# Kernel optimization log

Hardware: AMD Instinct MI355X
Metric: run time of the kernel (lower is better)

The kernel has to match this reference:

```python
import jax, jax.numpy as jnp
import numpy as np

LAYERS, HIDDEN, FFN, HEADS = 4, 128, 256, 4
HEAD_D = HIDDEN // HEADS          # 32
V_HEAD = 2 * HEAD_D               # 64 (double_v_dim)
V_DIM = 2 * HIDDEN                # 256
SCALE_BASE = 512
EPS = 1e-5
GAMMAS = (1.0 - np.exp(np.linspace(np.log(1.0 / 32), np.log(1.0 / 512), HEADS))).astype(np.float32)


def _xpos(x, downscale):
    # x: (..., L, d) -- xpos rotary embedding with per-position decay scale
    L, d = x.shape[-2], x.shape[-1]
    half = d // 2
    base_scale = (jnp.arange(half, dtype=jnp.float32) + 0.4 * d) / (1.4 * d)   # (half,)
    power = jnp.arange(L, dtype=jnp.float32)[:, None] / SCALE_BASE
    sc = base_scale[None, :] ** power                                          # (L, half)
    inv_freq = 1.0 / (10000.0 ** (jnp.arange(half, dtype=jnp.float32) / half))
    ang = jnp.arange(L, dtype=jnp.float32)[:, None] * inv_freq[None, :]        # (L, half)
    sin, cos = jnp.sin(ang), jnp.cos(ang)
    if downscale:
        sc = 1.0 / sc
    sin_d = jnp.repeat(sin * sc, 2, axis=-1)   # duplicate_interleave -> (L, d)
    cos_d = jnp.repeat(cos * sc, 2, axis=-1)
    x1, x2 = x[..., ::2], x[..., 1::2]
    rot = jnp.stack((-x2, x1), axis=-1).reshape(x.shape)  # rotate_every_two
    return x * cos_d + rot * sin_d


def _layer_norm(x, w, b):
    mu = x.mean(-1, keepdims=True)
    var = x.var(-1, keepdims=True)
    return (x - mu) / jnp.sqrt(var + EPS) * w + b


def _msr(X, wq, wk, wv, wg, wo, gn_w, gn_b):
    # MultiScaleRetention, parallel form. X: (B, L, HIDDEN)
    B, L, _ = X.shape
    Q = _xpos(jnp.einsum('blh,nhd->bnld', X, wq), False)   # (B, heads, L, 32)
    K = _xpos(jnp.einsum('blh,nhd->bnld', X, wk), True)
    V = jnp.einsum('blh,nhv->bnlv', X, wv)                 # (B, heads, L, 64)
    n = jnp.arange(L)
    diff = n[:, None] - n[None, :]
    gam = jnp.asarray(GAMMAS)[:, None, None]
    D = jnp.where(diff >= 0, gam ** jnp.maximum(diff, 0).astype(jnp.float32), 0.0)  # (heads, L, L)
    scores = jnp.einsum('bnld,bnmd->bnlm', Q, K) * D[None]
    Y = jnp.einsum('bnlm,bnmv->bnlv', scores, V)
    Y = Y.transpose(0, 2, 1, 3).reshape(B, L, V_DIM)       # concat heads on feature dim
    # GroupNorm(heads, V_DIM) over the channel axis
    Yg = Y.reshape(B, L, HEADS, V_HEAD)
    mu = Yg.mean(-1, keepdims=True)
    var = Yg.var(-1, keepdims=True)
    Yn = ((Yg - mu) / jnp.sqrt(var + EPS)).reshape(B, L, V_DIM) * gn_w + gn_b
    G = X @ wg
    return (G * jax.nn.sigmoid(G) * Yn) @ wo               # swish gate, output proj


def _forward(x, rem_w1, rem_b1, rem_w2, rem_b2, rem_w3, rem_b3,
             wq, wk, wv, wg, wo, gn_w, gn_b,
             ln1_w, ln1_b, ln2_w, ln2_b,
             ffn_w1, ffn_b1, ffn_w2, ffn_b2,
             dec_w1, dec_b1, dec_w2, dec_b2):
    gelu = lambda t: jax.nn.gelu(t, approximate=False)
    # REM: 5 -> 32 -> 64 -> 128, GELU after each linear
    X = gelu(gelu(gelu(x @ rem_w1 + rem_b1) @ rem_w2 + rem_b2) @ rem_w3 + rem_b3)
    # RetNet: pre-LN retention + pre-LN FFN blocks with residuals
    for i in range(LAYERS):
        Y = _msr(_layer_norm(X, ln1_w[i], ln1_b[i]), wq[i], wk[i], wv[i],
                 wg[i], wo[i], gn_w[i], gn_b[i]) + X
        Z = _layer_norm(Y, ln2_w[i], ln2_b[i])
        X = gelu(Z @ ffn_w1[i] + ffn_b1[i]) @ ffn_w2[i] + ffn_b2[i] + Y
    # Decoder: 128 -> 64 -> 20, softmax over classes
    logits = gelu(X @ dec_w1 + dec_b1) @ dec_w2 + dec_b2
    return jax.nn.softmax(logits, axis=-1)


def setup_inputs() -> dict:
    key = jax.random.key(0)
    ks = jax.random.split(key, 16)
    rn = lambda k, shape, s=0.02: jax.random.normal(k, shape, dtype=jnp.float32) * s
    B, L = 64, 512
    return {
        'x': jax.random.normal(ks[0], (B, L, 5), dtype=jnp.float32),
        'rem_w1': rn(ks[1], (5, 32)), 'rem_b1': jnp.zeros((32,), jnp.float32),
        'rem_w2': rn(ks[2], (32, 64)), 'rem_b2': jnp.zeros((64,), jnp.float32),
        'rem_w3': rn(ks[3], (64, HIDDEN)), 'rem_b3': jnp.zeros((HIDDEN,), jnp.float32),
        'wq': rn(ks[4], (LAYERS, HEADS, HIDDEN, HEAD_D), 1.0 / HIDDEN),
        'wk': rn(ks[5], (LAYERS, HEADS, HIDDEN, HEAD_D), 1.0 / HIDDEN),
        'wv': rn(ks[6], (LAYERS, HEADS, HIDDEN, V_HEAD), 1.0 / HIDDEN),
        'wg': rn(ks[7], (LAYERS, HIDDEN, V_DIM), 1.0 / HIDDEN),
        'wo': rn(ks[8], (LAYERS, V_DIM, HIDDEN), 1.0 / HIDDEN),
        'gn_w': jnp.ones((LAYERS, V_DIM), jnp.float32),
        'gn_b': jnp.zeros((LAYERS, V_DIM), jnp.float32),
        'ln1_w': jnp.ones((LAYERS, HIDDEN), jnp.float32),
        'ln1_b': jnp.zeros((LAYERS, HIDDEN), jnp.float32),
        'ln2_w': jnp.ones((LAYERS, HIDDEN), jnp.float32),
        'ln2_b': jnp.zeros((LAYERS, HIDDEN), jnp.float32),
        'ffn_w1': rn(ks[9], (LAYERS, HIDDEN, FFN)),
        'ffn_b1': jnp.zeros((LAYERS, FFN), jnp.float32),
        'ffn_w2': rn(ks[10], (LAYERS, FFN, HIDDEN)),
        'ffn_b2': jnp.zeros((LAYERS, HIDDEN), jnp.float32),
        'dec_w1': rn(ks[11], (HIDDEN, 64)), 'dec_b1': jnp.zeros((64,), jnp.float32),
        'dec_w2': rn(ks[12], (64, 20)), 'dec_b2': jnp.zeros((20,), jnp.float32),
    }


def reference(x, rem_w1, rem_b1, rem_w2, rem_b2, rem_w3, rem_b3,
              wq, wk, wv, wg, wo, gn_w, gn_b,
              ln1_w, ln1_b, ln2_w, ln2_b,
              ffn_w1, ffn_b1, ffn_w2, ffn_b2,
              dec_w1, dec_b1, dec_w2, dec_b2):
    return _forward(x, rem_w1, rem_b1, rem_w2, rem_b2, rem_w3, rem_b3,
                    wq, wk, wv, wg, wo, gn_w, gn_b,
                    ln1_w, ln1_b, ln2_w, ln2_b,
                    ffn_w1, ffn_b1, ffn_w2, ffn_b2,
                    dec_w1, dec_b1, dec_w2, dec_b2)
```

## Files before the change

kernel.cpp:

```cpp
#include <hip/hip_runtime.h>
#include <math.h>
#include <cmath>

#define SEQ   512
#define NBATCH 64
#define BT    32768
#define HID   128
#define NHEAD 4
#define HD    32
#define VHD   64
#define VDIM  256
#define FFND  256

typedef __attribute__((ext_vector_type(8))) short bf16x8;
typedef __attribute__((ext_vector_type(4))) float f32x4;
typedef unsigned short u16;

__device__ __forceinline__ float gelu_f(float x){ return 0.5f*x*(1.f+erff(x*0.70710678118f)); }

__device__ __forceinline__ u16 f2bf(float f){
  __bf16 h = (__bf16)f;
  union{__bf16 h; u16 u;} v; v.h = h; return v.u;
}
__device__ __forceinline__ float bf2f(u16 u){
  union{unsigned u; float f;} v; v.u = ((unsigned)u)<<16; return v.f;
}

__device__ __forceinline__ void gload16(const void* g, void* l){
  __builtin_amdgcn_global_load_lds(
      (const __attribute__((address_space(1))) unsigned*)g,
      (__attribute__((address_space(3))) unsigned*)l, 16, 0, 0);
}

#define STAGE_TILE_N(dst, base, strideU16, colOffU16, wid_, srow_, phys16l_, NIT) \
  do{                                                                           \
    _Pragma("unroll")                                                           \
    for(int it_=0; it_<NIT; it_++){                                             \
      int blk_ = (wid_)*NIT + it_;                                              \
      int row_ = blk_*4 + (srow_);                                              \
      int log16_ = (phys16l_) ^ (row_&15);                                      \
      gload16((base) + (size_t)row_*(strideU16) + (colOffU16) + log16_*8,       \
              &(dst)[blk_*512]);                                                \
    }                                                                           \
  }while(0)

#define STAGE_TILE(dst, base, strideU16, colOffU16, wid_, srow_, phys16l_) \
  STAGE_TILE_N(dst, base, strideU16, colOffU16, wid_, srow_, phys16l_, 8)

__global__ __launch_bounds__(256) void wconv_kernel(
    const float* __restrict__ wq, const float* __restrict__ wk,
    const float* __restrict__ wv, const float* __restrict__ wg,
    const float* __restrict__ wo, const float* __restrict__ f1,
    const float* __restrict__ f2, const float* __restrict__ dw1,
    const float* __restrict__ w2e, const float* __restrict__ w3e,
    u16* __restrict__ Wt)
{
  int idx = blockIdx.x*256 + threadIdx.x;
  if(idx >= 786432){
    int q = idx - 786432;
    if(q < 8192){ int col=q>>7, h=q&127; Wt[idx]=f2bf(dw1[h*64+col]); }
    else if(q < 10240){ int p=q-8192; int row=p>>5, col=p&31; Wt[idx]=f2bf(w2e[col*64+row]); }
    else { int p=q-10240; int row=p>>6, col=p&63; Wt[idx]=f2bf(w3e[col*128+row]); }
    return;
  }
  int layer = idx / 196608;
  int r = idx - layer*196608;
  u16* W = Wt + (size_t)layer*196608;
  const float* wq_l = wq + (size_t)layer*16384;
  const float* wk_l = wk + (size_t)layer*16384;
  const float* wv_l = wv + (size_t)layer*32768;
  const float* wg_l = wg + (size_t)layer*32768;
  const float* wo_l = wo + (size_t)layer*32768;
  const float* f1_l = f1 + (size_t)layer*32768;
  const float* f2_l = f2 + (size_t)layer*32768;
  float v;
  if(r < 98304){
    int col = r>>7, h = r&127;
    if(col<128){ int n=col>>5, d=col&31; v = wq_l[(n*128+h)*32+d]; }
    else if(col<256){ int c=col-128, n=c>>5, d=c&31; v = wk_l[(n*128+h)*32+d]; }
    else if(col<512){ int c=col-256, n=c>>6, j=c&63; v = wv_l[(n*128+h)*64+j]; }
    else { int p=col-512; v = wg_l[h*256+p]; }
    W[r] = f2bf(v);
  } else if(r < 131072){
    int q = r-98304; int col=q>>8, k=q&255;
    W[r] = f2bf(wo_l[k*128+col]);
  } else if(r < 163840){
    int q = r-131072; int col=q>>7, h=q&127;
    W[r] = f2bf(f1_l[h*256+col]);
  } else {
    int q = r-163840; int col=q>>8, k=q&255;
    W[r] = f2bf(f2_l[k*128+col]);
  }
}

__global__ __launch_bounds__(256) void embed_kernel(
    const float* __restrict__ x,
    const float* __restrict__ w1, const float* __restrict__ b1,
    const float* __restrict__ b2, const float* __restrict__ b3,
    const u16* __restrict__ W23t,
    const float* __restrict__ lnw, const float* __restrict__ lnb,
    float* __restrict__ X, u16* __restrict__ xn)
{
  __shared__ float sx[64][6];
  __shared__ float sw1[160], sb1[32], sb2[64], sb3[128];
  __shared__ u16 big[18944];
  int t=threadIdx.x, lane=t&63, wid=t>>6, mrow=lane&15, quad=lane>>4, r0=wid*16;
  int tok0=blockIdx.x*64;

  for(int i=t;i<320;i+=256) sx[i/5][i%5]=x[(size_t)tok0*5+i];
  for(int i=t;i<160;i+=256) sw1[i]=w1[i];
  if(t<32) sb1[t]=b1[t];
  if(t<64) sb2[t]=b2[t];
  if(t<128) sb3[t]=b3[t];
  for(int c=t;c<256;c+=256){ int row=c>>2, c8=(c&3)*8;
    *(uint4*)&big[2560+row*40+c8]=*(const uint4*)&W23t[row*32+c8]; }
  for(int c=t;c<1024;c+=256){ int row=c>>3, c8=(c&7)*8;
    *(uint4*)&big[9728+row*72+c8]=*(const uint4*)&W23t[2048+row*64+c8]; }
  __syncthreads();

  for(int task=t; task<2048; task+=256){
    int tok=task>>5, j=task&31;
    float a=sb1[j];
    #pragma unroll
    for(int i=0;i<5;i++) a+=sx[tok][i]*sw1[i*32+j];
    big[tok*40+j]=f2bf(gelu_f(a));
  }
  __syncthreads();

  f32x4 h2[4];
  #pragma unroll
  for(int cc=0;cc<4;cc++) h2[cc]=(f32x4){0.f,0.f,0.f,0.f};
  {
    bf16x8 a=*(const bf16x8*)&big[(r0+mrow)*40+quad*8];
    #pragma unroll
    for(int cc=0;cc<4;cc++){
      bf16x8 b=*(const bf16x8*)&big[2560+(cc*16+mrow)*40+quad*8];
      h2[cc]=__builtin_amdgcn_mfma_f32_16x16x32_bf16(a,b,h2[cc],0,0,0);
    }
  }
  #pragma unroll
  for(int cc=0;cc<4;cc++){
    float bs=sb2[cc*16+mrow];
    #pragma unroll
    for(int reg=0;reg<4;reg++)
      big[5120+(r0+quad*4+reg)*72+cc*16+mrow]=f2bf(gelu_f(h2[cc][reg]+bs));
  }
  __syncthreads();

  f32x4 xac[8];
  #pragma unroll
  for(int cc=0;cc<8;cc++) xac[cc]=(f32x4){0.f,0.f,0.f,0.f};
  #pragma unroll
  for(int ks=0;ks<2;ks++){
    bf16x8 a=*(const bf16x8*)&big[5120+(r0+mrow)*72+ks*32+quad*8];
    #pragma unroll
    for(int cc=0;cc<8;cc++){
      bf16x8 b=*(const bf16x8*)&big[9728+(cc*16+mrow)*72+ks*32+quad*8];
      xac[cc]=__builtin_amdgcn_mfma_f32_16x16x32_bf16(a,b,xac[cc],0,0,0);
    }
  }
  __syncthreads();

  #pragma unroll
  for(int reg=0;reg<4;reg++){
    int rowl=r0+quad*4+reg, rowg=tok0+rowl;
    float xv[8], s=0.f, sq=0.f;
    #pragma unroll
    for(int cc=0;cc<8;cc++){
      float v=gelu_f(xac[cc][reg]+sb3[cc*16+mrow]);
      xv[cc]=v; s+=v; sq+=v*v;
    }
    #pragma unroll
    for(int m=1;m<16;m<<=1){ s+=__shfl_xor(s,m); sq+=__shfl_xor(sq,m); }
    float mu=s*(1.f/128.f);
    float var=sq*(1.f/128.f)-mu*mu;
    float rstd=rsqrtf(var+1e-5f);
    #pragma unroll
    for(int cc=0;cc<8;cc++){
      int col=cc*16+mrow;
      X[(size_t)rowg*128+col]=xv[cc];
      big[rowl*136+col]=f2bf((xv[cc]-mu)*rstd*lnw[col]+lnb[col]);
    }
  }
  __syncthreads();
  for(int th=t; th<1024; th+=256){
    int row=th>>4, seg=th&15;
    *(uint4*)&xn[(size_t)(tok0+row)*128+seg*8]=*(const uint4*)&big[row*136+seg*8];
  }
}

__device__ __forceinline__ void qkvg_epilogue(
    int nc, f32x4 acc[2][4], u16* stg,
    int t, int mrow, int quad, int r0q, int c0q, int b, int l0, int tok0,
    u16* __restrict__ Q, u16* __restrict__ K,
    u16* __restrict__ Vt, u16* __restrict__ G)
{
  if(nc < 2){
    bool isK = (nc==1);
    float sgn = isK ? -1.f : 1.f;
    #pragma unroll
    for(int cc=0;cc<4;cc++){
      int colc = c0q + cc*16 + mrow;
      int i = (colc&31)>>1;
      float log2bs = log2f(((float)i + 12.8f)*(1.f/44.8f));
      float invf   = exp2f(-(float)i * (13.28771238f/16.f));
      float rstep  = exp2f(sgn*log2bs*(1.f/512.f));
      float c1 = cosf(invf), s1 = sinf(invf);
      #pragma unroll
      for(int rr=0;rr<2;rr++){
        int rowl0 = r0q + rr*16 + quad*4;
        float lb = (float)(l0 + rowl0);
        float sc = exp2f(sgn*log2bs*lb*(1.f/512.f));
        float ang = lb*invf;
        float u = cosf(ang)*sc, v = sinf(ang)*sc;
        #pragma unroll
        for(int reg=0;reg<4;reg++){
          int rowl = rowl0 + reg;
          float val = acc[rr][cc][reg];
          float partner = __shfl_xor(val, 1);
          float o = (colc&1) ? (val*u + partner*v) : (val*u - partner*v);
          stg[rowl*136 + colc] = f2bf(o);
          float un = (u*c1 - v*s1)*rstep;
          float vn = (u*s1 + v*c1)*rstep;
          u = un; v = vn;
        }
      }
    }
    __syncthreads();
    u16* O = isK ? K : Q;
    for(int th=t; th<1024; th+=256){
      int row=th>>4, n=(th>>2)&3, seg=th&3;
      *(uint4*)&O[(((size_t)(b*4+n)*512) + (l0+row))*32 + seg*8]
        = *(const uint4*)&stg[row*136 + n*32 + seg*8];
    }
  } else if(nc < 4){
    #pragma unroll
    for(int cc=0;cc<4;cc++){
      int colc = c0q + cc*16 + mrow;
      #pragma unroll
      for(int rr=0;rr<2;rr++){
        #pragma unroll
        for(int reg=0;reg<4;reg++){
          int rowl = r0q + rr*16 + quad*4 + reg;
          stg[colc*72 + rowl] = f2bf(acc[rr][cc][reg]);
        }
      }
    }
    __syncthreads();
    int jbase = (nc-2)*128;
    for(int th=t; th<1024; th+=256){
      int row=th>>3, seg=th&7;
      int jg = jbase + row; int n = jg>>6, j = jg&63;
      *(uint4*)&Vt[(((size_t)(b*4+n)*64) + j)*512 + l0 + seg*8]
        = *(const uint4*)&stg[row*72 + seg*8];
    }
  } else {
    #pragma unroll
    for(int cc=0;cc<4;cc++){
      int colc = c0q + cc*16 + mrow;
      #pragma unroll
      for(int rr=0;rr<2;rr++){
        #pragma unroll
        for(int reg=0;reg<4;reg++){
          int rowl = r0q + rr*16 + quad*4 + reg;
          stg[rowl*136 + colc] = f2bf(acc[rr][cc][reg]);
        }
      }
    }
    __syncthreads();
    int gc0 = (nc-4)*128;
    for(int th=t; th<1024; th+=256){
      int row=th>>4, seg=th&15;
      *(uint4*)&G[((size_t)(tok0+row))*256 + gc0 + seg*8]
        = *(const uint4*)&stg[row*136 + seg*8];
    }
  }
}

__device__ __forceinline__ void qkvg_epi8(
    int nc, f32x4 acc[4], u16* stg,
    int t, int mrow, int quad, int r0, int c0, int b, int l0, int tok0,
    u16* __restrict__ Q, u16* __restrict__ K,
    u16* __restrict__ Vt, u16* __restrict__ G)
{
  if(nc < 2){
    bool isK = (nc==1);
    float sgn = isK ? -1.f : 1.f;
    #pragma unroll
    for(int cc=0;cc<4;cc++){
      int colc = c0 + cc*16 + mrow;
      int i = (colc&31)>>1;
      float log2bs = log2f(((float)i + 12.8f)*(1.f/44.8f));
      float invf   = exp2f(-(float)i * (13.28771238f/16.f));
      float rstep  = exp2f(sgn*log2bs*(1.f/512.f));
      float c1 = cosf(invf), s1 = sinf(invf);
      int rowl0 = r0 + quad*4;
      float lb = (float)(l0 + rowl0);
      float sc = exp2f(sgn*log2bs*lb*(1.f/512.f));
      float ang = lb*invf;
      float u = cosf(ang)*sc, v = sinf(ang)*sc;
      #pragma unroll
      for(int reg=0;reg<4;reg++){
        int rowl = rowl0 + reg;
        float val = acc[cc][reg];
        float partner = __shfl_xor(val, 1);
        float o = (colc&1) ? (val*u + partner*v) : (val*u - partner*v);
        stg[rowl*136 + colc] = f2bf(o);
        float un = (u*c1 - v*s1)*rstep;
        float vn = (u*s1 + v*c1)*rstep;
        u = un; v = vn;
      }
    }
    __syncthreads();
    u16* O = isK ? K : Q;
    for(int th=t; th<1024; th+=512){
      int row=th>>4, n=(th>>2)&3, seg=th&3;
      *(uint4*)&O[(((size_t)(b*4+n)*512) + (l0+row))*32 + seg*8]
        = *(const uint4*)&stg[row*136 + n*32 + seg*8];
    }
  } else if(nc < 4){
    #pragma unroll
    for(int cc=0;cc<4;cc++){
      int colc = c0 + cc*16 + mrow;
      #pragma unroll
      for(int reg=0;reg<4;reg++){
        int rowl = r0 + quad*4 + reg;
        stg[colc*72 + rowl] = f2bf(acc[cc][reg]);
      }
    }
    __syncthreads();
    int jbase = (nc-2)*128;
    for(int th=t; th<1024; th+=512){
      int row=th>>3, seg=th&7;
      int jg = jbase + row; int n = jg>>6, j = jg&63;
      *(uint4*)&Vt[(((size_t)(b*4+n)*64) + j)*512 + l0 + seg*8]
        = *(const uint4*)&stg[row*72 + seg*8];
    }
  } else {
    #pragma unroll
    for(int cc=0;cc<4;cc++){
      int colc = c0 + cc*16 + mrow;
      #pragma unroll
      for(int reg=0;reg<4;reg++){
        int rowl = r0 + quad*4 + reg;
        stg[rowl*136 + colc] = f2bf(acc[cc][reg]);
      }
    }
    __syncthreads();
    int gc0 = (nc-4)*128;
    for(int th=t; th<1024; th+=512){
      int row=th>>4, seg=th&15;
      *(uint4*)&G[((size_t)(tok0+row))*256 + gc0 + seg*8]
        = *(const uint4*)&stg[row*136 + seg*8];
    }
  }
}

__global__ __launch_bounds__(256) void qkvg_kernel(
    const u16* __restrict__ A, const u16* __restrict__ Wt,
    u16* __restrict__ Q, u16* __restrict__ K,
    u16* __restrict__ Vt, u16* __restrict__ G)
{
  __shared__ u16 sW[128*128];
  u16* stg = sW;
  int t = threadIdx.x, lane = t&63, wid = t>>6;
  int mrow = lane&15, quad = lane>>4;
  int srow = lane>>4, phys16l = lane&15;
  int r0q = (wid>>1)*32, c0q = (wid&1)*64;
  int tok0 = blockIdx.x*64;
  int b = tok0>>9, l0 = tok0&511;

  bf16x8 a0f[4], a1f[4];
  #pragma unroll
  for(int ks=0; ks<4; ks++){
    a0f[ks] = *(const bf16x8*)&A[(size_t)(tok0+r0q+mrow)*128 + ks*32+quad*8];
    a1f[ks] = *(const bf16x8*)&A[(size_t)(tok0+r0q+16+mrow)*128 + ks*32+quad*8];
  }

  for(int ch=0; ch<3; ch++){
    int nc = blockIdx.y*3 + ch;
    if(ch) __syncthreads();
    STAGE_TILE(sW, Wt + (size_t)nc*16384, 128, 0, wid, srow, phys16l);
    __syncthreads();

    f32x4 acc[2][4];
    #pragma unroll
    for(int rr=0;rr<2;rr++)
      #pragma unroll
      for(int cc=0;cc<4;cc++) acc[rr][cc] = (f32x4){0.f,0.f,0.f,0.f};
    #pragma unroll
    for(int ks=0; ks<4; ks++){
      #pragma unroll
      for(int cc=0; cc<4; cc++){
        bf16x8 bb = *(const bf16x8*)&sW[(c0q+cc*16+mrow)*128 + (((ks*4+quad)^mrow)<<3)];
        acc[0][cc] = __builtin_amdgcn_mfma_f32_16x16x32_bf16(a0f[ks],bb,acc[0][cc],0,0,0);
        acc[1][cc] = __builtin_amdgcn_mfma_f32_16x16x32_bf16(a1f[ks],bb,acc[1][cc],0,0,0);
      }
    }
    __syncthreads();
    qkvg_epilogue(nc, acc, stg, t, mrow, quad, r0q, c0q, b, l0, tok0, Q, K, Vt, G);
  }
}

__global__ __launch_bounds__(512, 4) void mlpq_kernel(
    const u16* __restrict__ Gated, const u16* __restrict__ Wo,
    const u16* __restrict__ W1t, const float* __restrict__ b1,
    const u16* __restrict__ W2t, const float* __restrict__ b2,
    const float* __restrict__ Xin,
    const float* __restrict__ ln2w, const float* __restrict__ ln2b,
    const float* __restrict__ ln1w, const float* __restrict__ ln1b,
    float* __restrict__ Xout,
    const u16* __restrict__ Wq,
    u16* __restrict__ Q, u16* __restrict__ K,
    u16* __restrict__ Vt, u16* __restrict__ G)
{
  __shared__ u16 sW[32768];
  __shared__ float sRed[64][2][2];
  u16* bufA = sW;
  u16* bufB = sW + 16384;
  int t=threadIdx.x, lane=t&63, wid=t>>6, mrow=lane&15, quad=lane>>4;
  int rg=wid>>1, half=wid&1;
  int r0=rg*16, c0=half*64;
  int tok0=blockIdx.x*64;
  int srow = lane>>4, phys16l = lane&15;

  STAGE_TILE_N(bufA, Wo, 256, 0, wid, srow, phys16l, 4);
  bf16x8 gfrag[8];
  #pragma unroll
  for(int ks=0;ks<8;ks++)
    gfrag[ks]=*(const bf16x8*)&Gated[(size_t)(tok0+r0+mrow)*256 + ks*32+quad*8];
  __syncthreads();

  STAGE_TILE_N(bufB, Wo, 256, 128, wid, srow, phys16l, 4);
  f32x4 yac[4];
  #pragma unroll
  for(int cc=0;cc<4;cc++) yac[cc]=(f32x4){0.f,0.f,0.f,0.f};
  #pragma unroll
  for(int cc=0;cc<4;cc++){
    #pragma unroll
    for(int ks=0;ks<4;ks++){
      bf16x8 b=*(const bf16x8*)&bufA[(c0+cc*16+mrow)*128 + (((ks*4+quad)^mrow)<<3)];
      yac[cc]=__builtin_amdgcn_mfma_f32_16x16x32_bf16(gfrag[ks],b,yac[cc],0,0,0);
    }
  }
  __syncthreads();

  STAGE_TILE_N(bufA, W1t, 128, 0, wid, srow, phys16l, 4);
  #pragma unroll
  for(int cc=0;cc<4;cc++){
    #pragma unroll
    for(int ks=0;ks<4;ks++){
      bf16x8 b=*(const bf16x8*)&bufB[(c0+cc*16+mrow)*128 + (((ks*4+quad)^mrow)<<3)];
      yac[cc]=__builtin_amdgcn_mfma_f32_16x16x32_bf16(gfrag[4+ks],b,yac[cc],0,0,0);
    }
  }
  float yv[4][4];
  #pragma unroll
  for(int reg=0;reg<4;reg++){
    int rowl=r0+quad*4+reg, rowg=tok0+rowl;
    float s=0.f, sq=0.f;
    #pragma unroll
    for(int cc=0;cc<4;cc++){
      float v=yac[cc][reg]+Xin[(size_t)rowg*128+c0+cc*16+mrow];
      yv[cc][reg]=v; s+=v; sq+=v*v;
    }
    #pragma unroll
    for(int m=1;m<16;m<<=1){ s+=__shfl_xor(s,m); sq+=__shfl_xor(sq,m); }
    if(mrow==0){ sRed[rowl][half][0]=s; sRed[rowl][half][1]=sq; }
  }
  __syncthreads();

  #pragma unroll
  for(int reg=0;reg<4;reg++){
    int rowl=r0+quad*4+reg;
    float s =sRed[rowl][0][0]+sRed[rowl][1][0];
    float sq=sRed[rowl][0][1]+sRed[rowl][1][1];
    float mu=s*(1.f/128.f);
    float var=sq*(1.f/128.f)-mu*mu;
    float rstd=rsqrtf(var+1e-5f);
    #pragma unroll
    for(int cc=0;cc<4;cc++){
      int col=c0+cc*16+mrow;
      bufB[rowl*136+col]=f2bf((yv[cc][reg]-mu)*rstd*ln2w[col]+ln2b[col]);
    }
  }
  __syncthreads();
  bf16x8 az[4];
  #pragma unroll
  for(int ks=0;ks<4;ks++) az[ks]=*(const bf16x8*)&bufB[(r0+mrow)*136+ks*32+quad*8];
  __syncthreads();

  bf16x8 hfrag[8];
  STAGE_TILE_N(bufB, W1t + (size_t)16384, 128, 0, wid, srow, phys16l, 4);
  {
    f32x4 hac[4];
    #pragma unroll
    for(int cc=0;cc<4;cc++) hac[cc]=(f32x4){0.f,0.f,0.f,0.f};
    #pragma unroll
    for(int cc=0;cc<4;cc++){
      #pragma unroll
      for(int ks=0;ks<4;ks++){
        bf16x8 b=*(const bf16x8*)&bufA[(c0+cc*16+mrow)*128 + (((ks*4+quad)^mrow)<<3)];
        hac[cc]=__builtin_amdgcn_mfma_f32_16x16x32_bf16(az[ks],b,hac[cc],0,0,0);
      }
    }
    __syncthreads();
    #pragma unroll
    for(int cc=0;cc<4;cc++){
      float bs=b1[c0+cc*16+mrow];
      #pragma unroll
      for(int reg=0;reg<4;reg++)
        bufA[(r0+quad*4+reg)*136 + c0+cc*16+mrow]=f2bf(gelu_f(hac[cc][reg]+bs));
    }
    __syncthreads();
    #pragma unroll
    for(int ks=0;ks<4;ks++) hfrag[ks]=*(const bf16x8*)&bufA[(r0+mrow)*136+ks*32+quad*8];
    __syncthreads();
  }

  STAGE_TILE_N(bufA, W2t, 256, 0, wid, srow, phys16l, 4);
  {
    f32x4 hac[4];
    #pragma unroll
    for(int cc=0;cc<4;cc++) hac[cc]=(f32x4){0.f,0.f,0.f,0.f};
    #pragma unroll
    for(int cc=0;cc<4;cc++){
      #pragma unroll
      for(int ks=0;ks<4;ks++){
        bf16x8 b=*(const bf16x8*)&bufB[(c0+cc*16+mrow)*128 + (((ks*4+quad)^mrow)<<3)];
        hac[cc]=__builtin_amdgcn_mfma_f32_16x16x32_bf16(az[ks],b,hac[cc],0,0,0);
      }
    }
    __syncthreads();
    #pragma unroll
    for(int cc=0;cc<4;cc++){
      float bs=b1[128+c0+cc*16+mrow];
      #pragma unroll
      for(int reg=0;reg<4;reg++)
        bufB[(r0+quad*4+reg)*136 + c0+cc*16+mrow]=f2bf(gelu_f(hac[cc][reg]+bs));
    }
    __syncthreads();
    #pragma unroll
    for(int ks=0;ks<4;ks++) hfrag[4+ks]=*(const bf16x8*)&bufB[(r0+mrow)*136+ks*32+quad*8];
    __syncthreads();
  }

  STAGE_TILE_N(bufB, W2t, 256, 128, wid, srow, phys16l, 4);
  f32x4 xac[4];
  #pragma unroll
  for(int cc=0;cc<4;cc++) xac[cc]=(f32x4){0.f,0.f,0.f,0.f};
  #pragma unroll
  for(int cc=0;cc<4;cc++){
    #pragma unroll
    for(int ks=0;ks<4;ks++){
      bf16x8 b=*(const bf16x8*)&bufA[(c0+cc*16+mrow)*128 + (((ks*4+quad)^mrow)<<3)];
      xac[cc]=__builtin_amdgcn_mfma_f32_16x16x32_bf16(hfrag[ks],b,xac[cc],0,0,0);
    }
  }
  __syncthreads();

  if(Wq) STAGE_TILE_N(bufA, Wq, 128, 0, wid, srow, phys16l, 4);
  #pragma unroll
  for(int cc=0;cc<4;cc++){
    #pragma unroll
    for(int ks=0;ks<4;ks++){
      bf16x8 b=*(const bf16x8*)&bufB[(c0+cc*16+mrow)*128 + (((ks*4+quad)^mrow)<<3)];
      xac[cc]=__builtin_amdgcn_mfma_f32_16x16x32_bf16(hfrag[4+ks],b,xac[cc],0,0,0);
    }
  }
  float xv[4][4];
  #pragma unroll
  for(int reg=0;reg<4;reg++){
    int rowl=r0+quad*4+reg;
    float s=0.f, sq=0.f;
    #pragma unroll
    for(int cc=0;cc<4;cc++){
      float v=xac[cc][reg]+b2[c0+cc*16+mrow]+yv[cc][reg];
      xv[cc][reg]=v; s+=v; sq+=v*v;
    }
    #pragma unroll
    for(int m=1;m<16;m<<=1){ s+=__shfl_xor(s,m); sq+=__shfl_xor(sq,m); }
    if(mrow==0){ sRed[rowl][half][0]=s; sRed[rowl][half][1]=sq; }
  }
  __syncthreads();

  #pragma unroll
  for(int reg=0;reg<4;reg++){
    int rowl=r0+quad*4+reg, rowg=tok0+rowl;
    float s =sRed[rowl][0][0]+sRed[rowl][1][0];
    float sq=sRed[rowl][0][1]+sRed[rowl][1][1];
    float mu=s*(1.f/128.f);
    float var=sq*(1.f/128.f)-mu*mu;
    float rstd=rsqrtf(var+1e-5f);
    #pragma unroll
    for(int cc=0;cc<4;cc++){
      int col=c0+cc*16+mrow;
      Xout[(size_t)rowg*128+col]=xv[cc][reg];
      if(Wq) bufB[rowl*136+col]=f2bf((xv[cc][reg]-mu)*rstd*ln1w[col]+ln1b[col]);
    }
  }
  if(!Wq) return;
  __syncthreads();
  bf16x8 aq[4];
  #pragma unroll
  for(int ks=0; ks<4; ks++)
    aq[ks] = *(const bf16x8*)&bufB[(r0+mrow)*136 + ks*32+quad*8];
  __syncthreads();

  int b = tok0>>9, l0 = tok0&511;
  for(int nc=0; nc<6; nc++){
    u16* cur = (nc&1) ? bufB : bufA;
    u16* nxt = (nc&1) ? bufA : bufB;
    if(nc<5) STAGE_TILE_N(nxt, Wq + (size_t)(nc+1)*16384, 128, 0, wid, srow, phys16l, 4);

    f32x4 acc[4];
    #pragma unroll
    for(int cc=0;cc<4;cc++) acc[cc] = (f32x4){0.f,0.f,0.f,0.f};
    #pragma unroll
    for(int ks=0; ks<4; ks++){
      #pragma unroll
      for(int cc=0; cc<4; cc++){
        bf16x8 bb = *(const bf16x8*)&cur[(c0+cc*16+mrow)*128 + (((ks*4+quad)^mrow)<<3)];
        acc[cc] = __builtin_amdgcn_mfma_f32_16x16x32_bf16(aq[ks],bb,acc[cc],0,0,0);
      }
    }
    __syncthreads();
    qkvg_epi8(nc, acc, cur, t, mrow, quad, r0, c0, b, l0, tok0, Q, K, Vt, G);
    __syncthreads();
  }
}

__global__ __launch_bounds__(256) void retmfma_kernel(
    const u16* __restrict__ Q, const u16* __restrict__ K,
    const u16* __restrict__ Vt, const u16* __restrict__ G,
    const float* __restrict__ gnw, const float* __restrict__ gnb,
    u16* __restrict__ Gated, float4 log2g)
{
  int idx = blockIdx.x;
  int bn = ((idx>>6)<<3) | (idx&7);
  int lt = (idx>>3)&7;
  int n = bn & 3, b = bn >> 2;
  float lg2g = (n==0)?log2g.x:(n==1)?log2g.y:(n==2)?log2g.z:log2g.w;
  __shared__ u16 sK[64][40];
  __shared__ u16 sVt[64][72];
  __shared__ u16 sS[64][72];
  int t = threadIdx.x, lane = t&63, wid = t>>6;
  int mrow = lane&15, quad = lane>>4;
  int r0 = wid*16;

  bf16x8 qa = *(const bf16x8*)&Q[((size_t)bn*512 + lt*64 + r0+mrow)*32 + quad*8];

  f32x4 oacc[4];
  #pragma unroll
  for(int cc=0;cc<4;cc++) oacc[cc] = (f32x4){0.f,0.f,0.f,0.f};
  float gp1 = exp2f(lg2g), gp2 = gp1*gp1, gp3 = gp2*gp1;
  float gpow[4] = {1.f, gp1, gp2, gp3};
  float gw[4], gb[4];
  #pragma unroll
  for(int cc=0;cc<4;cc++){ gw[cc]=gnw[n*64+cc*16+mrow]; gb[cc]=gnb[n*64+cc*16+mrow]; }
  int rowl0 = lt*64 + r0 + quad*4;

  int krow = t>>2, kc8 = (t&3)*8;
  int vrow = t>>3, vc8 = (t&7)*8;
  const u16* Kb = K  + ((size_t)bn*512 + krow)*32 + kc8;
  const u16* V0 = Vt + ((size_t)bn*64 + vrow)*512 + vc8;
  const u16* V1 = Vt + ((size_t)bn*64 + vrow+32)*512 + vc8;
  uint4 ldk  = *(const uint4*)(Kb);
  uint4 ldv0 = *(const uint4*)(V0);
  uint4 ldv1 = *(const uint4*)(V1);

  for(int mt=0; mt<=lt; mt++){
    if(mt) __syncthreads();
    *(uint4*)&sK[krow][kc8]     = ldk;
    *(uint4*)&sVt[vrow][vc8]    = ldv0;
    *(uint4*)&sVt[vrow+32][vc8] = ldv1;
    if(mt < lt){
      ldk  = *(const uint4*)(Kb + (size_t)(mt+1)*2048);
      ldv0 = *(const uint4*)(V0 + (mt+1)*64);
      ldv1 = *(const uint4*)(V1 + (mt+1)*64);
    }
    __syncthreads();
    f32x4 sacc[4];
    #pragma unroll
    for(int cc=0;cc<4;cc++){
      bf16x8 bb = *(const bf16x8*)&sK[cc*16+mrow][quad*8];
      sacc[cc] = __builtin_amdgcn_mfma_f32_16x16x32_bf16(qa,bb,(f32x4){0.f,0.f,0.f,0.f},0,0,0);
    }
    #pragma unroll
    for(int cc=0;cc<4;cc++){
      int colm = mt*64 + cc*16 + mrow;
      int d0 = rowl0 - colm;
      float w0 = exp2f(lg2g*(float)d0);
      #pragma unroll
      for(int reg=0;reg<4;reg++){
        float w = (d0+reg>=0) ? w0*gpow[reg] : 0.f;
        sS[r0+quad*4+reg][cc*16+mrow] = f2bf(sacc[cc][reg]*w);
      }
    }
    __syncthreads();
    #pragma unroll
    for(int ks=0;ks<2;ks++){
      bf16x8 a = *(const bf16x8*)&sS[r0+mrow][ks*32+quad*8];
      #pragma unroll
      for(int cc=0;cc<4;cc++){
        bf16x8 bb = *(const bf16x8*)&sVt[cc*16+mrow][ks*32+quad*8];
        oacc[cc] = __builtin_amdgcn_mfma_f32_16x16x32_bf16(a,bb,oacc[cc],0,0,0);
      }
    }
  }

  __syncthreads();
  #pragma unroll
  for(int reg=0;reg<4;reg++){
    float s=0.f, sq=0.f;
    #pragma unroll
    for(int cc=0;cc<4;cc++){ float v=oacc[cc][reg]; s+=v; sq+=v*v; }
    #pragma unroll
    for(int m=1;m<16;m<<=1){ s+=__shfl_xor(s,m); sq+=__shfl_xor(sq,m); }
    float mu = s*(1.f/64.f);
    float var = sq*(1.f/64.f) - mu*mu;
    float rn = rsqrtf(var + 1e-5f);
    int rowl = r0 + quad*4 + reg;
    int l = lt*64 + rowl;
    size_t gbase = ((size_t)(b*512 + l))*256 + n*64;
    #pragma unroll
    for(int cc=0;cc<4;cc++){
      float gg = bf2f(G[gbase + cc*16+mrow]);
      float gate = gg/(1.f+expf(-gg));
      sS[rowl][cc*16+mrow] = f2bf(gate*((oacc[cc][reg]-mu)*rn*gw[cc] + gb[cc]));
    }
  }
  __syncthreads();
  for(int th=t; th<512; th+=256){
    int row=th>>3, seg=th&7;
    *(uint4*)&Gated[((size_t)(b*512 + lt*64 + row))*256 + n*64 + seg*8]
      = *(const uint4*)&sS[row][seg*8];
  }
}

__global__ __launch_bounds__(256) void dec_kernel(
    const float* __restrict__ X, const u16* __restrict__ W1t,
    const float* __restrict__ b1, const float* __restrict__ w2,
    const float* __restrict__ b2, float* __restrict__ out)
{
  __shared__ u16 sA[64][136];
  __shared__ u16 sW[64][136];
  __shared__ float sH[64][68];
  __shared__ float sL[64*20];
  __shared__ float sw2[64*20];
  __shared__ float sb2[20];
  int t = threadIdx.x, lane = t&63, wid = t>>6;
  int mrow = lane&15, quad = lane>>4;
  int tok0 = blockIdx.x*64;

  for(int th=t; th<2048; th+=256){
    int row=th>>5, c4=(th&31)*4;
    float4 v = *(const float4*)&X[(size_t)(tok0+row)*128 + c4];
    ushort4 p; p.x=f2bf(v.x); p.y=f2bf(v.y); p.z=f2bf(v.z); p.w=f2bf(v.w);
    *(ushort4*)&sA[row][c4] = p;
  }
  for(int th=t; th<1024; th+=256){
    int row=th>>4, c8=(th&15)*8;
    *(uint4*)&sW[row][c8] = *(const uint4*)&W1t[(size_t)row*128 + c8];
  }
  for(int i=t;i<1280;i+=256) sw2[i]=w2[i];
  if(t<20) sb2[t]=b2[t];
  __syncthreads();

  int r0 = wid*16;
  f32x4 acc[4];
  #pragma unroll
  for(int cc=0;cc<4;cc++) acc[cc] = (f32x4){0.f,0.f,0.f,0.f};
  #pragma unroll
  for(int ks=0; ks<4; ks++){
    int koff = ks*32 + quad*8;
    bf16x8 a = *(const bf16x8*)&sA[r0+mrow][koff];
    #pragma unroll
    for(int cc=0; cc<4; cc++){
      bf16x8 b = *(const bf16x8*)&sW[cc*16+mrow][koff];
      acc[cc] = __builtin_amdgcn_mfma_f32_16x16x32_bf16(a,b,acc[cc],0,0,0);
    }
  }
  #pragma unroll
  for(int cc=0;cc<4;cc++){
    int col = cc*16 + mrow;
    float bb = b1[col];
    #pragma unroll
    for(int reg=0;reg<4;reg++){
      sH[r0 + quad*4 + reg][col] = gelu_f(acc[cc][reg] + bb);
    }
  }
  __syncthreads();

  for(int task=t; task<1280; task+=256){
    int tk = task/20, o = task - tk*20;
    float a = sb2[o];
    for(int k=0;k<64;k++) a += sH[tk][k]*sw2[k*20+o];
    sL[tk*20+o] = a;
  }
  __syncthreads();
  if(t < 64){
    float mx = -1e30f;
    #pragma unroll
    for(int o=0;o<20;o++) mx = fmaxf(mx, sL[t*20+o]);
    float sum = 0.f;
    float e[20];
    #pragma unroll
    for(int o=0;o<20;o++){ e[o]=expf(sL[t*20+o]-mx); sum += e[o]; }
    float inv = 1.f/sum;
    #pragma unroll
    for(int o=0;o<20;o++) sL[t*20+o] = e[o]*inv;
  }
  __syncthreads();
  for(int th=t; th<1280; th+=256){
    out[(size_t)tok0*20 + th] = sL[th];
  }
}

extern "C" void kernel_launch(void* const* d_in, const int* in_sizes, int n_in,
                              void* d_out, int out_size, void* d_ws, size_t ws_size,
                              hipStream_t stream) {
  (void)in_sizes; (void)n_in; (void)out_size; (void)ws_size;
  const float* x      = (const float*)d_in[0];
  const float* rem_w1 = (const float*)d_in[1];
  const float* rem_b1 = (const float*)d_in[2];
  const float* rem_w2 = (const float*)d_in[3];
  const float* rem_b2 = (const float*)d_in[4];
  const float* rem_w3 = (const float*)d_in[5];
  const float* rem_b3 = (const float*)d_in[6];
  const float* wq     = (const float*)d_in[7];
  const float* wk     = (const float*)d_in[8];
  const float* wv     = (const float*)d_in[9];
  const float* wg     = (const float*)d_in[10];
  const float* wo     = (const float*)d_in[11];
  const float* gn_w   = (const float*)d_in[12];
  const float* gn_b   = (const float*)d_in[13];
  const float* ln1_w  = (const float*)d_in[14];
  const float* ln1_b  = (const float*)d_in[15];
  const float* ln2_w  = (const float*)d_in[16];
  const float* ln2_b  = (const float*)d_in[17];
  const float* ffn_w1 = (const float*)d_in[18];
  const float* ffn_b1 = (const float*)d_in[19];
  const float* ffn_w2 = (const float*)d_in[20];
  const float* ffn_b2 = (const float*)d_in[21];
  const float* dec_w1 = (const float*)d_in[22];
  const float* dec_b1 = (const float*)d_in[23];
  const float* dec_w2 = (const float*)d_in[24];
  const float* dec_b2 = (const float*)d_in[25];
  float* outp = (float*)d_out;

  const size_t S128 = (size_t)BT*128;
  const size_t S256 = (size_t)BT*256;
  float* ws = (float*)d_ws;
  float* Xb = ws;
  u16*  Qb16    = (u16*)(Xb + S128);
  u16*  Kb16    = Qb16 + (size_t)BT*32;
  u16*  Vt16    = Kb16 + (size_t)BT*32;
  u16*  XnBf    = Vt16 + (size_t)BT*64;
  u16*  GBf     = XnBf + S128;
  u16*  GatedBf = GBf + S256;
  u16*  WtBf    = GatedBf + S256;

  double lgA = log(1.0/32.0), lgB = log(1.0/512.0);
  float4 l2g;
  {
    double g0 = 1.0 - exp(lgA + 0.0*(lgB-lgA)/3.0);
    double g1 = 1.0 - exp(lgA + 1.0*(lgB-lgA)/3.0);
    double g2 = 1.0 - exp(lgA + 2.0*(lgB-lgA)/3.0);
    double g3 = 1.0 - exp(lgA + 3.0*(lgB-lgA)/3.0);
    l2g.x = (float)(log(g0)/log(2.0));
    l2g.y = (float)(log(g1)/log(2.0));
    l2g.z = (float)(log(g2)/log(2.0));
    l2g.w = (float)(log(g3)/log(2.0));
  }

  wconv_kernel<<<3144, 256, 0, stream>>>(wq, wk, wv, wg, wo, ffn_w1, ffn_w2, dec_w1,
                                         rem_w2, rem_w3, WtBf);
  embed_kernel<<<BT/64, 256, 0, stream>>>(x, rem_w1, rem_b1, rem_b2, rem_b3,
                                          WtBf+794624, ln1_w, ln1_b, Xb, XnBf);
  qkvg_kernel<<<dim3(BT/64,2), 256, 0, stream>>>(XnBf, WtBf, Qb16, Kb16, Vt16, GBf);

  for(int li=0; li<4; li++){
    u16* Wt_l = WtBf + (size_t)li*196608;
    const float* gnw_l = gn_w + (size_t)li*VDIM;
    const float* gnb_l = gn_b + (size_t)li*VDIM;
    const float* l2w = ln2_w + (size_t)li*HID, *l2b = ln2_b + (size_t)li*HID;
    const float* f1b = ffn_b1 + (size_t)li*FFND;
    const float* f2b = ffn_b2 + (size_t)li*HID;
    int nli = (li+1)&3;
    const float* n1w = ln1_w + (size_t)nli*HID, *n1b = ln1_b + (size_t)nli*HID;
    const u16* Wq_next = (li<3) ? (WtBf + (size_t)(li+1)*196608) : nullptr;

    retmfma_kernel<<<2048, 256, 0, stream>>>(Qb16, Kb16, Vt16, GBf, gnw_l, gnb_l, GatedBf, l2g);
    mlpq_kernel<<<BT/64, 512, 0, stream>>>(
        GatedBf, Wt_l+98304, Wt_l+131072, f1b, Wt_l+163840, f2b,
        Xb, l2w, l2b, n1w, n1b, Xb,
        Wq_next, Qb16, Kb16, Vt16, GBf);
  }

  dec_kernel<<<BT/64, 256, 0, stream>>>(Xb, WtBf+786432, dec_b1, dec_w2, dec_b2, outp);
}
```

Baseline: 449.4 us.

## Fuse retention into the per-layer MLP/QKV kernel with ping-pong QKVG buffers

Folds the retention attention computation into the layer kernel. Each 512-thread block processes all four heads for its 64-token tile, two heads at a time across its two 256-thread halves, and keeps the gated retention output in registers as MFMA fragments instead of writing it to global memory and reading it back. Q/K/Vt/G are double-buffered across layers, because other blocks still read the current layer's K/V while this layer writes the next one. This removes one kernel launch per layer and the Gated round trip. In exchange, blocks on later tiles do up to 8 causal inner iterations while early ones do one, so load is imbalanced, and there is less parallelism than the previous 2048-block retention grid.

```diff
diff --git a/kernel.cpp b/kernel.cpp
--- a/kernel.cpp
+++ b/kernel.cpp
@@ -402,8 +402,11 @@
   }
 }
 
-__global__ __launch_bounds__(512, 4) void mlpq_kernel(
-    const u16* __restrict__ Gated, const u16* __restrict__ Wo,
+__global__ __launch_bounds__(512, 4) void layer_kernel(
+    const u16* __restrict__ Qin, const u16* __restrict__ Kin,
+    const u16* __restrict__ Vtin, const u16* __restrict__ Gin,
+    const float* __restrict__ gnw, const float* __restrict__ gnb, float4 l2g,
+    const u16* __restrict__ Wo,
     const u16* __restrict__ W1t, const float* __restrict__ b1,
     const u16* __restrict__ W2t, const float* __restrict__ b2,
     const float* __restrict__ Xin,
@@ -411,24 +414,129 @@
     const float* __restrict__ ln1w, const float* __restrict__ ln1b,
     float* __restrict__ Xout,
     const u16* __restrict__ Wq,
-    u16* __restrict__ Q, u16* __restrict__ K,
-    u16* __restrict__ Vt, u16* __restrict__ G)
+    u16* __restrict__ Qo, u16* __restrict__ Ko,
+    u16* __restrict__ Vto, u16* __restrict__ Go)
 {
-  __shared__ u16 sW[32768];
-  __shared__ float sRed[64][2][2];
-  u16* bufA = sW;
-  u16* bufB = sW + 16384;
+  __shared__ u16 smem[33280];
+  u16* bufA = smem;
+  u16* bufB = smem + 16384;
+  float (*sRed)[2][2] = (float(*)[2][2])(smem + 32768);
   int t=threadIdx.x, lane=t&63, wid=t>>6, mrow=lane&15, quad=lane>>4;
   int rg=wid>>1, half=wid&1;
   int r0=rg*16, c0=half*64;
   int tok0=blockIdx.x*64;
   int srow = lane>>4, phys16l = lane&15;
 
+  int half8 = wid>>2, lw = wid&3;
+  int tl = t & 255;
+  int r0l = lw*16;
+  int lt = (tok0>>6)&7;
+  int bq = tok0>>9;
+  bf16x8 gfrag[8];
+
+  #pragma unroll
+  for(int p=0;p<2;p++){
+    int n = 2*p + half8;
+    int bn = bq*4 + n;
+    float lg2g = (n==0)?l2g.x:(n==1)?l2g.y:(n==2)?l2g.z:l2g.w;
+    u16* rK = smem + half8*11776;
+    u16* rV = rK + 2560;
+    u16* rS = rK + 7168;
+
+    bf16x8 qa = *(const bf16x8*)&Qin[((size_t)bn*512 + lt*64 + r0l+mrow)*32 + quad*8];
+    f32x4 oacc[4];
+    #pragma unroll
+    for(int cc=0;cc<4;cc++) oacc[cc] = (f32x4){0.f,0.f,0.f,0.f};
+    float gp1 = exp2f(lg2g), gp2 = gp1*gp1, gp3 = gp2*gp1;
+    float gpow[4] = {1.f, gp1, gp2, gp3};
+    float gw[4], gb[4];
+    #pragma unroll
+    for(int cc=0;cc<4;cc++){ gw[cc]=gnw[n*64+cc*16+mrow]; gb[cc]=gnb[n*64+cc*16+mrow]; }
+    int rowl0 = lt*64 + r0l + quad*4;
+
+    int krow = tl>>2, kc8 = (tl&3)*8;
+    int vrow = tl>>3, vc8 = (tl&7)*8;
+    const u16* Kb = Kin  + ((size_t)bn*512 + krow)*32 + kc8;
+    const u16* V0 = Vtin + ((size_t)bn*64 + vrow)*512 + vc8;
+    const u16* V1 = Vtin + ((size_t)bn*64 + vrow+32)*512 + vc8;
+    uint4 ldk  = *(const uint4*)(Kb);
+    uint4 ldv0 = *(const uint4*)(V0);
+    uint4 ldv1 = *(const uint4*)(V1);
+
+    for(int mt=0; mt<=lt; mt++){
+      if(mt) __syncthreads();
+      *(uint4*)&rK[krow*40+kc8]      = ldk;
+      *(uint4*)&rV[vrow*72+vc8]      = ldv0;
+      *(uint4*)&rV[(vrow+32)*72+vc8] = ldv1;
+      if(mt < lt){
+        ldk  = *(const uint4*)(Kb + (size_t)(mt+1)*2048);
+        ldv0 = *(const uint4*)(V0 + (mt+1)*64);
+        ldv1 = *(const uint4*)(V1 + (mt+1)*64);
+      }
+      __syncthreads();
+      f32x4 sacc[4];
+      #pragma unroll
+      for(int cc=0;cc<4;cc++){
+        bf16x8 bb = *(const bf16x8*)&rK[(cc*16+mrow)*40 + quad*8];
+        sacc[cc] = __builtin_amdgcn_mfma_f32_16x16x32_bf16(qa,bb,(f32x4){0.f,0.f,0.f,0.f},0,0,0);
+      }
+      #pragma unroll
+      for(int cc=0;cc<4;cc++){
+        int colm = mt*64 + cc*16 + mrow;
+        int d0 = rowl0 - colm;
+        float w0 = exp2f(lg2g*(float)d0);
+        #pragma unroll
+        for(int reg=0;reg<4;reg++){
+          float w = (d0+reg>=0) ? w0*gpow[reg] : 0.f;
+          rS[(r0l+quad*4+reg)*72 + cc*16+mrow] = f2bf(sacc[cc][reg]*w);
+        }
+      }
+      __syncthreads();
+      #pragma unroll
+      for(int ks=0;ks<2;ks++){
+        bf16x8 a = *(const bf16x8*)&rS[(r0l+mrow)*72 + ks*32+quad*8];
+        #pragma unroll
+        for(int cc=0;cc<4;cc++){
+          bf16x8 bb = *(const bf16x8*)&rV[(cc*16+mrow)*72 + ks*32+quad*8];
+          oacc[cc] = __builtin_amdgcn_mfma_f32_16x16x32_bf16(a,bb,oacc[cc],0,0,0);
+        }
+      }
+    }
+
+    __syncthreads();
+    #pragma unroll
+    for(int reg=0;reg<4;reg++){
+      float s=0.f, sq=0.f;
+      #pragma unroll
+      for(int cc=0;cc<4;cc++){ float v=oacc[cc][reg]; s+=v; sq+=v*v; }
+      #pragma unroll
+      for(int m=1;m<16;m<<=1){ s+=__shfl_xor(s,m); sq+=__shfl_xor(sq,m); }
+      float mu = s*(1.f/64.f);
+      float var = sq*(1.f/64.f) - mu*mu;
+      float rn = rsqrtf(var + 1e-5f);
+      int rowl = r0l + quad*4 + reg;
+      int l = lt*64 + rowl;
+      size_t gbase = ((size_t)(bq*512 + l))*256 + n*64;
+      #pragma unroll
+      for(int cc=0;cc<4;cc++){
+        float gg = bf2f(Gin[gbase + cc*16+mrow]);
+        float gate = gg/(1.f+expf(-gg));
+        rS[rowl*72 + cc*16+mrow] = f2bf(gate*((oacc[cc][reg]-mu)*rn*gw[cc] + gb[cc]));
+      }
+    }
+    __syncthreads();
+    #pragma unroll
+    for(int hh=0; hh<2; hh++){
+      int nn = 2*p + hh;
+      const u16* src = smem + hh*11776 + 7168;
+      #pragma unroll
+      for(int ksl=0; ksl<2; ksl++)
+        gfrag[2*nn+ksl] = *(const bf16x8*)&src[(r0+mrow)*72 + ksl*32 + quad*8];
+    }
+    __syncthreads();
+  }
+
   STAGE_TILE_N(bufA, Wo, 256, 0, wid, srow, phys16l, 4);
-  bf16x8 gfrag[8];
-  #pragma unroll
-  for(int ks=0;ks<8;ks++)
-    gfrag[ks]=*(const bf16x8*)&Gated[(size_t)(tok0+r0+mrow)*256 + ks*32+quad*8];
   __syncthreads();
 
   STAGE_TILE_N(bufB, Wo, 256, 128, wid, srow, phys16l, 4);
@@ -625,116 +733,8 @@
       }
     }
     __syncthreads();
-    qkvg_epi8(nc, acc, cur, t, mrow, quad, r0, c0, b, l0, tok0, Q, K, Vt, G);
-    __syncthreads();
-  }
-}
-
-__global__ __launch_bounds__(256) void retmfma_kernel(
-    const u16* __restrict__ Q, const u16* __restrict__ K,
-    const u16* __restrict__ Vt, const u16* __restrict__ G,
-    const float* __restrict__ gnw, const float* __restrict__ gnb,
-    u16* __restrict__ Gated, float4 log2g)
-{
-  int idx = blockIdx.x;
-  int bn = ((idx>>6)<<3) | (idx&7);
-  int lt = (idx>>3)&7;
-  int n = bn & 3, b = bn >> 2;
-  float lg2g = (n==0)?log2g.x:(n==1)?log2g.y:(n==2)?log2g.z:log2g.w;
-  __shared__ u16 sK[64][40];
-  __shared__ u16 sVt[64][72];
-  __shared__ u16 sS[64][72];
-  int t = threadIdx.x, lane = t&63, wid = t>>6;
-  int mrow = lane&15, quad = lane>>4;
-  int r0 = wid*16;
-
-  bf16x8 qa = *(const bf16x8*)&Q[((size_t)bn*512 + lt*64 + r0+mrow)*32 + quad*8];
-
-  f32x4 oacc[4];
-  #pragma unroll
-  for(int cc=0;cc<4;cc++) oacc[cc] = (f32x4){0.f,0.f,0.f,0.f};
-  float gp1 = exp2f(lg2g), gp2 = gp1*gp1, gp3 = gp2*gp1;
-  float gpow[4] = {1.f, gp1, gp2, gp3};
-  float gw[4], gb[4];
-  #pragma unroll
-  for(int cc=0;cc<4;cc++){ gw[cc]=gnw[n*64+cc*16+mrow]; gb[cc]=gnb[n*64+cc*16+mrow]; }
-  int rowl0 = lt*64 + r0 + quad*4;
-
-  int krow = t>>2, kc8 = (t&3)*8;
-  int vrow = t>>3, vc8 = (t&7)*8;
-  const u16* Kb = K  + ((size_t)bn*512 + krow)*32 + kc8;
-  const u16* V0 = Vt + ((size_t)bn*64 + vrow)*512 + vc8;
-  const u16* V1 = Vt + ((size_t)bn*64 + vrow+32)*512 + vc8;
-  uint4 ldk  = *(const uint4*)(Kb);
-  uint4 ldv0 = *(const uint4*)(V0);
-  uint4 ldv1 = *(const uint4*)(V1);
-
-  for(int mt=0; mt<=lt; mt++){
-    if(mt) __syncthreads();
-    *(uint4*)&sK[krow][kc8]     = ldk;
-    *(uint4*)&sVt[vrow][vc8]    = ldv0;
-    *(uint4*)&sVt[vrow+32][vc8] = ldv1;
-    if(mt < lt){
-      ldk  = *(const uint4*)(Kb + (size_t)(mt+1)*2048);
-      ldv0 = *(const uint4*)(V0 + (mt+1)*64);
-      ldv1 = *(const uint4*)(V1 + (mt+1)*64);
-    }
-    __syncthreads();
-    f32x4 sacc[4];
-    #pragma unroll
-    for(int cc=0;cc<4;cc++){
-      bf16x8 bb = *(const bf16x8*)&sK[cc*16+mrow][quad*8];
-      sacc[cc] = __builtin_amdgcn_mfma_f32_16x16x32_bf16(qa,bb,(f32x4){0.f,0.f,0.f,0.f},0,0,0);
-    }
-    #pragma unroll
-    for(int cc=0;cc<4;cc++){
-      int colm = mt*64 + cc*16 + mrow;
-      int d0 = rowl0 - colm;
-      float w0 = exp2f(lg2g*(float)d0);
-      #pragma unroll
-      for(int reg=0;reg<4;reg++){
-        float w = (d0+reg>=0) ? w0*gpow[reg] : 0.f;
-        sS[r0+quad*4+reg][cc*16+mrow] = f2bf(sacc[cc][reg]*w);
-      }
-    }
-    __syncthreads();
-    #pragma unroll
-    for(int ks=0;ks<2;ks++){
-      bf16x8 a = *(const bf16x8*)&sS[r0+mrow][ks*32+quad*8];
-      #pragma unroll
-      for(int cc=0;cc<4;cc++){
-        bf16x8 bb = *(const bf16x8*)&sVt[cc*16+mrow][ks*32+quad*8];
-        oacc[cc] = __builtin_amdgcn_mfma_f32_16x16x32_bf16(a,bb,oacc[cc],0,0,0);
-      }
-    }
-  }
-
-  __syncthreads();
-  #pragma unroll
-  for(int reg=0;reg<4;reg++){
-    float s=0.f, sq=0.f;
-    #pragma unroll
-    for(int cc=0;cc<4;cc++){ float v=oacc[cc][reg]; s+=v; sq+=v*v; }
-    #pragma unroll
-    for(int m=1;m<16;m<<=1){ s+=__shfl_xor(s,m); sq+=__shfl_xor(sq,m); }
-    float mu = s*(1.f/64.f);
-    float var = sq*(1.f/64.f) - mu*mu;
-    float rn = rsqrtf(var + 1e-5f);
-    int rowl = r0 + quad*4 + reg;
-    int l = lt*64 + rowl;
-    size_t gbase = ((size_t)(b*512 + l))*256 + n*64;
-    #pragma unroll
-    for(int cc=0;cc<4;cc++){
-      float gg = bf2f(G[gbase + cc*16+mrow]);
-      float gate = gg/(1.f+expf(-gg));
-      sS[rowl][cc*16+mrow] = f2bf(gate*((oacc[cc][reg]-mu)*rn*gw[cc] + gb[cc]));
-    }
-  }
-  __syncthreads();
-  for(int th=t; th<512; th+=256){
-    int row=th>>3, seg=th&7;
-    *(uint4*)&Gated[((size_t)(b*512 + lt*64 + row))*256 + n*64 + seg*8]
-      = *(const uint4*)&sS[row][seg*8];
+    qkvg_epi8(nc, acc, cur, t, mrow, quad, r0, c0, b, l0, tok0, Qo, Ko, Vto, Go);
+    __syncthreads();
   }
 }
 
@@ -853,13 +853,16 @@
   const size_t S256 = (size_t)BT*256;
   float* ws = (float*)d_ws;
   float* Xb = ws;
-  u16*  Qb16    = (u16*)(Xb + S128);
-  u16*  Kb16    = Qb16 + (size_t)BT*32;
-  u16*  Vt16    = Kb16 + (size_t)BT*32;
-  u16*  XnBf    = Vt16 + (size_t)BT*64;
-  u16*  GBf     = XnBf + S128;
-  u16*  GatedBf = GBf + S256;
-  u16*  WtBf    = GatedBf + S256;
+  u16*  Q0  = (u16*)(Xb + S128);
+  u16*  K0  = Q0 + (size_t)BT*32;
+  u16*  Vt0 = K0 + (size_t)BT*32;
+  u16*  Q1  = Vt0 + (size_t)BT*64;
+  u16*  K1  = Q1 + (size_t)BT*32;
+  u16*  Vt1 = K1 + (size_t)BT*32;
+  u16*  XnBf = Q1;
+  u16*  G0  = Vt1 + (size_t)BT*64;
+  u16*  G1  = G0 + S256;
+  u16*  WtBf = G1 + S256;
 
   double lgA = log(1.0/32.0), lgB = log(1.0/512.0);
   float4 l2g;
@@ -878,7 +881,7 @@
                                          rem_w2, rem_w3, WtBf);
   embed_kernel<<<BT/64, 256, 0, stream>>>(x, rem_w1, rem_b1, rem_b2, rem_b3,
                                           WtBf+794624, ln1_w, ln1_b, Xb, XnBf);
-  qkvg_kernel<<<dim3(BT/64,2), 256, 0, stream>>>(XnBf, WtBf, Qb16, Kb16, Vt16, GBf);
+  qkvg_kernel<<<dim3(BT/64,2), 256, 0, stream>>>(XnBf, WtBf, Q0, K0, Vt0, G0);
 
   for(int li=0; li<4; li++){
     u16* Wt_l = WtBf + (size_t)li*196608;
@@ -891,11 +894,20 @@
     const float* n1w = ln1_w + (size_t)nli*HID, *n1b = ln1_b + (size_t)nli*HID;
     const u16* Wq_next = (li<3) ? (WtBf + (size_t)(li+1)*196608) : nullptr;
 
-    retmfma_kernel<<<2048, 256, 0, stream>>>(Qb16, Kb16, Vt16, GBf, gnw_l, gnb_l, GatedBf, l2g);
-    mlpq_kernel<<<BT/64, 512, 0, stream>>>(
-        GatedBf, Wt_l+98304, Wt_l+131072, f1b, Wt_l+163840, f2b,
+    const u16* Qi  = (li&1) ? Q1  : Q0;
+    const u16* Ki  = (li&1) ? K1  : K0;
+    const u16* Vti = (li&1) ? Vt1 : Vt0;
+    const u16* Gi  = (li&1) ? G1  : G0;
+    u16* Qo  = (li&1) ? Q0  : Q1;
+    u16* Ko  = (li&1) ? K0  : K1;
+    u16* Vto = (li&1) ? Vt0 : Vt1;
+    u16* Go  = (li&1) ? G0  : G1;
+
+    layer_kernel<<<BT/64, 512, 0, stream>>>(
+        Qi, Ki, Vti, Gi, gnw_l, gnb_l, l2g,
+        Wt_l+98304, Wt_l+131072, f1b, Wt_l+163840, f2b,
         Xb, l2w, l2b, n1w, n1b, Xb,
-        Wq_next, Qb16, Kb16, Vt16, GBf);
+        Wq_next, Qo, Ko, Vto, Go);
   }
 
   dec_kernel<<<BT/64, 256, 0, stream>>>(Xb, WtBf+786432, dec_b1, dec_w2, dec_b2, outp);
```

New measurement: 452.2 us. About the same (+0.6%).
